# Kernel optimization log

Hardware: AMD Instinct MI355X
Metric: run time of the kernel (lower is better)

## Reference

```python
import jax, jax.numpy as jnp
import numpy as np

N_QUBITS = 4
N_LAYERS = 2
DIM = 2 ** N_QUBITS
B, S, E = 4, 512, 512


def _apply_ry_batched(state, theta, wire):
    # per-element RY data-encoding; state: [N, 2,2,2,2], theta: [N]
    ax = wire + 1
    half = theta * 0.5
    bshape = (-1,) + (1,) * (N_QUBITS - 1)
    c = jnp.cos(half).reshape(bshape)
    s = jnp.sin(half).reshape(bshape)
    s0 = jnp.take(state, 0, axis=ax)
    s1 = jnp.take(state, 1, axis=ax)
    return jnp.stack([c * s0 - s * s1, s * s0 + c * s1], axis=ax)


def _rot_gate(w3):
    # combined RZ(c) @ RY(b) @ RX(a), 2x2 complex (applied RX first)
    a, b, c = w3[0] * 0.5, w3[1] * 0.5, w3[2] * 0.5
    ca, sa = jnp.cos(a), jnp.sin(a)
    cb, sb = jnp.cos(b), jnp.sin(b)
    RX = jnp.array([[ca + 0j, -1j * sa], [-1j * sa, ca + 0j]])
    RY = jnp.array([[cb + 0j, -sb + 0j], [sb + 0j, cb + 0j]])
    ez = jnp.exp(-1j * c)
    RZ = jnp.array([[ez, 0j], [0j, jnp.conj(ez)]])
    return (RZ @ RY @ RX).astype(jnp.complex64)


def _apply_gate(state, gate, wire):
    s = jnp.tensordot(state, gate, axes=([wire + 1], [1]))
    return jnp.moveaxis(s, -1, wire + 1)


def _apply_cnot(state, ctrl, tgt):
    s = jnp.moveaxis(state, (ctrl + 1, tgt + 1), (1, 2))
    s = jnp.stack([s[:, 0], s[:, 1, ::-1]], axis=1)
    return jnp.moveaxis(s, (1, 2), (ctrl + 1, tgt + 1))


def _quantum_scores(angles, weights):
    # angles: [N, N_QUBITS] real; returns [N] = sum_i <Z_i>
    n = angles.shape[0]
    state = jnp.zeros((n, DIM), jnp.complex64).at[:, 0].set(1.0)
    state = state.reshape((n,) + (2,) * N_QUBITS)
    for w in range(N_QUBITS):
        state = _apply_ry_batched(state, angles[:, w], w)
    wmat = weights.reshape(N_LAYERS, N_QUBITS, 3)
    for layer in range(N_LAYERS):
        for w in range(N_QUBITS):
            state = _apply_gate(state, _rot_gate(wmat[layer, w]), w)
        for w in range(N_QUBITS - 1):
            state = _apply_cnot(state, w, w + 1)
        if N_QUBITS > 2:
            state = _apply_cnot(state, N_QUBITS - 1, 0)
    probs = (state.real ** 2 + state.imag ** 2).reshape(n, DIM)
    idx = np.arange(DIM)
    bits = (idx[:, None] >> np.arange(N_QUBITS)) & 1  # [DIM, n_qubits]
    zvec = jnp.asarray((1 - 2 * bits).sum(axis=1), jnp.float32)  # sum_i (-1)^bit_i
    return probs @ zvec


def setup_inputs() -> dict:
    key = jax.random.key(0)
    ks = jax.random.split(key, 8)
    x = jax.random.normal(ks[0], (B, S, E), jnp.float32)
    def lin(kk, fi, fo):
        return jax.random.normal(kk, (fi, fo), jnp.float32) / np.sqrt(fi)
    Wq = lin(ks[1], E, N_QUBITS)
    Wk = lin(ks[2], E, N_QUBITS)
    Wv = lin(ks[3], E, N_QUBITS)
    Wout = lin(ks[4], N_QUBITS, E)
    bq = 0.1 * jax.random.normal(ks[5], (N_QUBITS,), jnp.float32)
    bk = 0.1 * jax.random.normal(ks[6], (N_QUBITS,), jnp.float32)
    bv = jnp.zeros((N_QUBITS,), jnp.float32)
    bout = jnp.zeros((E,), jnp.float32)
    quantum_weights = 0.1 * jax.random.normal(ks[7], (N_LAYERS * N_QUBITS * 3,), jnp.float32)
    return {"x": x, "Wq": Wq, "bq": bq, "Wk": Wk, "bk": bk, "Wv": Wv, "bv": bv,
            "quantum_weights": quantum_weights, "Wout": Wout, "bout": bout}


def reference(x, Wq, bq, Wk, bk, Wv, bv, quantum_weights, Wout, bout):
    b, s, e = x.shape
    q = jnp.tanh(x @ Wq + bq)          # [B,S,nq]
    k = jnp.tanh(x @ Wk + bk)          # [B,S,nq]
    v = x @ Wv + bv                    # [B,S,nq]
    # pairwise circuit inputs: tanh(q_i + k_j) for all (b,i,j)
    angles = jnp.tanh(q[:, :, None, :] + k[:, None, :, :]).reshape(-1, N_QUBITS)
    scores = _quantum_scores(angles, quantum_weights).reshape(b, s, s)
    attn = jax.nn.softmax(scores / np.sqrt(N_QUBITS), axis=-1)
    attended = jnp.einsum('bij,bjd->bid', attn, v)
    out = attended @ Wout + bout       # [B,S,E]
    return out, attn
```

## Files before the change

kernel.cpp:

```cpp
#include <hip/hip_runtime.h>
#include <math.h>

#define NQ 4
#define DIM 16
#define BB 4
#define SS 512
#define EE 512
#define ROWS (BB * SS)

__global__ __launch_bounds__(256) void k_prep(
    const float* __restrict__ x,
    const float* __restrict__ Wq, const float* __restrict__ bq,
    const float* __restrict__ Wk, const float* __restrict__ bk,
    const float* __restrict__ Wv, const float* __restrict__ bv,
    const float* __restrict__ qw,
    float* __restrict__ tq, float* __restrict__ tk, float* __restrict__ v,
    float* __restrict__ T_out) {
    if (blockIdx.x == 0) {
        __shared__ float sG[8][8];
        __shared__ float Ur[DIM][DIM];
        __shared__ float Ui[DIM][DIM];
        __shared__ float sMr[256];
        int t = threadIdx.x;
        if (t < 8) {
            float a = qw[t * 3 + 0] * 0.5f;
            float b = qw[t * 3 + 1] * 0.5f;
            float c = qw[t * 3 + 2] * 0.5f;
            float sa = __sinf(a), ca = __cosf(a);
            float sb = __sinf(b), cb = __cosf(b);
            float sc = __sinf(c), cc = __cosf(c);
            float m00r = cb * ca, m00i = sb * sa;
            float m01r = -sb * ca, m01i = -cb * sa;
            float m10r = sb * ca, m10i = -cb * sa;
            float m11r = cb * ca, m11i = -sb * sa;
            sG[t][0] = cc * m00r + sc * m00i;
            sG[t][1] = cc * m00i - sc * m00r;
            sG[t][2] = cc * m01r + sc * m01i;
            sG[t][3] = cc * m01i - sc * m01r;
            sG[t][4] = cc * m10r - sc * m10i;
            sG[t][5] = cc * m10i + sc * m10r;
            sG[t][6] = cc * m11r - sc * m11i;
            sG[t][7] = cc * m11i + sc * m11r;
        }
        __syncthreads();
        if (t < DIM) {
            float vr[DIM], vi[DIM];
#pragma unroll
            for (int i = 0; i < DIM; ++i) { vr[i] = (i == t) ? 1.f : 0.f; vi[i] = 0.f; }
#pragma unroll
            for (int gi = 0; gi < 8; ++gi) {
                int w = gi & 3;
                float g00r = sG[gi][0], g00i = sG[gi][1];
                float g01r = sG[gi][2], g01i = sG[gi][3];
                float g10r = sG[gi][4], g10i = sG[gi][5];
                float g11r = sG[gi][6], g11i = sG[gi][7];
                int mask = 1 << (3 - w);
#pragma unroll
                for (int idx = 0; idx < DIM; ++idx) {
                    if (idx & mask) continue;
                    int i1 = idx | mask;
                    float r0 = vr[idx], i0 = vi[idx], r1 = vr[i1], i1v = vi[i1];
                    vr[idx] = g00r * r0 - g00i * i0 + g01r * r1 - g01i * i1v;
                    vi[idx] = g00r * i0 + g00i * r0 + g01r * i1v + g01i * r1;
                    vr[i1]  = g10r * r0 - g10i * i0 + g11r * r1 - g11i * i1v;
                    vi[i1]  = g10r * i0 + g10i * r0 + g11r * i1v + g11i * r1;
                }
                if (w == 3) {
                    const int cwire[4] = {0, 1, 2, 3};
                    const int twire[4] = {1, 2, 3, 0};
#pragma unroll
                    for (int e = 0; e < 4; ++e) {
                        int cmask = 1 << (3 - cwire[e]);
                        int tmask = 1 << (3 - twire[e]);
                        float nr[DIM], ni[DIM];
#pragma unroll
                        for (int idx = 0; idx < DIM; ++idx) {
                            int src = (idx & cmask) ? (idx ^ tmask) : idx;
                            nr[idx] = vr[src]; ni[idx] = vi[src];
                        }
#pragma unroll
                        for (int idx = 0; idx < DIM; ++idx) { vr[idx] = nr[idx]; vi[idx] = ni[idx]; }
                    }
                }
            }
#pragma unroll
            for (int i = 0; i < DIM; ++i) { Ur[i][t] = vr[i]; Ui[i][t] = vi[i]; }
        }
        __syncthreads();
        {
            int k = t >> 4, l = t & 15;
            float acc = 0.f;
#pragma unroll
            for (int idx = 0; idx < DIM; ++idx) {
                float z = 4.f - 2.f * (float)__popc(idx);
                acc += z * (Ur[idx][k] * Ur[idx][l] + Ui[idx][k] * Ui[idx][l]);
            }
            sMr[t] = acc;
        }
        __syncthreads();
        if (t < 81) {
            int e3 = t % 3, e2 = (t / 3) % 3, e1 = (t / 9) % 3, e0 = t / 27;
            int xm = ((e0 == 2) << 3) | ((e1 == 2) << 2) | ((e2 == 2) << 1) | (int)(e3 == 2);
            int sm = ((e0 == 1) << 3) | ((e1 == 1) << 2) | ((e2 == 1) << 1) | (int)(e3 == 1);
            float acc = 0.f;
#pragma unroll
            for (int K = 0; K < DIM; ++K) {
                float s = (__popc(K & sm) & 1) ? -1.f : 1.f;
                acc += s * sMr[K * 16 + (K ^ xm)];
            }
            T_out[((e0 * 3 + e1) * 3 + e2) * 4 + e3] = acc * (1.f / 32.f);
        }
        if (t < 27) T_out[t * 4 + 3] = 0.f;
    } else {
        int row = (blockIdx.x - 1) * 4 + (threadIdx.x >> 6);
        int lane = threadIdx.x & 63;
        const float4* xr4 = (const float4*)(x + (size_t)row * EE);
        float aq[4] = {0, 0, 0, 0}, ak[4] = {0, 0, 0, 0}, av[4] = {0, 0, 0, 0};
#pragma unroll
        for (int h = 0; h < 2; ++h) {
            int e4 = lane + h * 64;
            float4 xv = xr4[e4];
            float xc[4] = {xv.x, xv.y, xv.z, xv.w};
#pragma unroll
            for (int c = 0; c < 4; ++c) {
                int e = e4 * 4 + c;
                float4 wq = *(const float4*)(Wq + e * 4);
                float4 wk = *(const float4*)(Wk + e * 4);
                float4 wv = *(const float4*)(Wv + e * 4);
                aq[0] = fmaf(xc[c], wq.x, aq[0]); aq[1] = fmaf(xc[c], wq.y, aq[1]);
                aq[2] = fmaf(xc[c], wq.z, aq[2]); aq[3] = fmaf(xc[c], wq.w, aq[3]);
                ak[0] = fmaf(xc[c], wk.x, ak[0]); ak[1] = fmaf(xc[c], wk.y, ak[1]);
                ak[2] = fmaf(xc[c], wk.z, ak[2]); ak[3] = fmaf(xc[c], wk.w, ak[3]);
                av[0] = fmaf(xc[c], wv.x, av[0]); av[1] = fmaf(xc[c], wv.y, av[1]);
                av[2] = fmaf(xc[c], wv.z, av[2]); av[3] = fmaf(xc[c], wv.w, av[3]);
            }
        }
#pragma unroll
        for (int off = 32; off > 0; off >>= 1) {
#pragma unroll
            for (int c = 0; c < 4; ++c) {
                aq[c] += __shfl_down(aq[c], off, 64);
                ak[c] += __shfl_down(ak[c], off, 64);
                av[c] += __shfl_down(av[c], off, 64);
            }
        }
        if (lane == 0) {
#pragma unroll
            for (int c = 0; c < 4; ++c) {
                tq[row * 4 + c] = tanhf(tanhf(aq[c] + bq[c]));
                tk[row * 4 + c] = tanhf(tanhf(ak[c] + bk[c]));
                v[row * 4 + c] = av[c] + bv[c];
            }
        }
    }
}

__global__ __launch_bounds__(256) void k_attn(
    const float* __restrict__ tq, const float* __restrict__ tk,
    const float* __restrict__ v, const float* __restrict__ Tg,
    const float* __restrict__ Wout, const float* __restrict__ bout,
    float* __restrict__ attn_out, float* __restrict__ out) {
    int row = blockIdx.x;
    int b = row >> 9;
    int tid = threadIdx.x;
    int wid = tid >> 6, lane = tid & 63;
    int j0 = tid, j1 = tid + 256;

    __shared__ float4 sT[27];
    __shared__ float red[4][5];

    if (tid < 27) sT[tid] = ((const float4*)Tg)[tid];
    __syncthreads();

    const float4 q4 = *(const float4*)(tq + row * 4);
    const float4 ka = *(const float4*)(tk + (size_t)(b * SS + j0) * 4);
    const float4 kb = *(const float4*)(tk + (size_t)(b * SS + j1) * 4);

    float t0a = (q4.x + ka.x) / fmaf(q4.x, ka.x, 1.f);
    float t1a = (q4.y + ka.y) / fmaf(q4.y, ka.y, 1.f);
    float t2a = (q4.z + ka.z) / fmaf(q4.z, ka.z, 1.f);
    float t3a = (q4.w + ka.w) / fmaf(q4.w, ka.w, 1.f);
    float t0b = (q4.x + kb.x) / fmaf(q4.x, kb.x, 1.f);
    float t1b = (q4.y + kb.y) / fmaf(q4.y, kb.y, 1.f);
    float t2b = (q4.z + kb.z) / fmaf(q4.z, kb.z, 1.f);
    float t3b = (q4.w + kb.w) / fmaf(q4.w, kb.w, 1.f);

    float c0a = __cosf(t0a), s0a = __sinf(t0a);
    float c1a = __cosf(t1a), s1a = __sinf(t1a);
    float c2a = __cosf(t2a), s2a = __sinf(t2a);
    float c3a = __cosf(t3a), s3a = __sinf(t3a);
    float c0b = __cosf(t0b), s0b = __sinf(t0b);
    float c1b = __cosf(t1b), s1b = __sinf(t1b);
    float c2b = __cosf(t2b), s2b = __sinf(t2b);
    float c3b = __cosf(t3b), s3b = __sinf(t3b);

    float u0a[3] = {1.f, c0a, s0a}, u1a[3] = {1.f, c1a, s1a}, u2a[3] = {1.f, c2a, s2a};
    float u0b[3] = {1.f, c0b, s0b}, u1b[3] = {1.f, c1b, s1b}, u2b[3] = {1.f, c2b, s2b};

    float sc_a = 0.f, sc_b = 0.f;
#pragma unroll
    for (int e0 = 0; e0 < 3; ++e0) {
        float a1a = 0.f, a1b = 0.f;
#pragma unroll
        for (int e1 = 0; e1 < 3; ++e1) {
            float a2a = 0.f, a2b = 0.f;
#pragma unroll
            for (int e2 = 0; e2 < 3; ++e2) {
                float4 Tv = sT[(e0 * 3 + e1) * 3 + e2];
                float ia = fmaf(s3a, Tv.z, fmaf(c3a, Tv.y, Tv.x));
                float ib = fmaf(s3b, Tv.z, fmaf(c3b, Tv.y, Tv.x));
                a2a = fmaf(u2a[e2], ia, a2a);
                a2b = fmaf(u2b[e2], ib, a2b);
            }
            a1a = fmaf(u1a[e1], a2a, a1a);
            a1b = fmaf(u1b[e1], a2b, a1b);
        }
        sc_a = fmaf(u0a[e0], a1a, sc_a);
        sc_b = fmaf(u0b[e0], a1b, sc_b);
    }

    float ex_a = __expf(sc_a);
    float ex_b = __expf(sc_b);

    const float4 va = *(const float4*)(v + (size_t)(b * SS + j0) * 4);
    const float4 vb = *(const float4*)(v + (size_t)(b * SS + j1) * 4);
    float vals[5];
    vals[0] = ex_a + ex_b;
    vals[1] = fmaf(ex_a, va.x, ex_b * vb.x);
    vals[2] = fmaf(ex_a, va.y, ex_b * vb.y);
    vals[3] = fmaf(ex_a, va.z, ex_b * vb.z);
    vals[4] = fmaf(ex_a, va.w, ex_b * vb.w);
#pragma unroll
    for (int off = 32; off > 0; off >>= 1) {
#pragma unroll
        for (int c = 0; c < 5; ++c) vals[c] += __shfl_xor(vals[c], off, 64);
    }
    if (lane == 0) {
#pragma unroll
        for (int c = 0; c < 5; ++c) red[wid][c] = vals[c];
    }
    __syncthreads();

    float tot = red[0][0] + red[1][0] + red[2][0] + red[3][0];
    float inv = 1.f / tot;

    attn_out[(size_t)row * SS + j0] = ex_a * inv;
    attn_out[(size_t)row * SS + j1] = ex_b * inv;

    float a0 = (red[0][1] + red[1][1] + red[2][1] + red[3][1]) * inv;
    float a1 = (red[0][2] + red[1][2] + red[2][2] + red[3][2]) * inv;
    float a2 = (red[0][3] + red[1][3] + red[2][3] + red[3][3]) * inv;
    float a3 = (red[0][4] + red[1][4] + red[2][4] + red[3][4]) * inv;

    int e = tid * 2;
    float2 w0 = *(const float2*)(Wout + 0 * EE + e);
    float2 w1 = *(const float2*)(Wout + 1 * EE + e);
    float2 w2 = *(const float2*)(Wout + 2 * EE + e);
    float2 w3 = *(const float2*)(Wout + 3 * EE + e);
    float2 bb = *(const float2*)(bout + e);
    float2 o;
    o.x = fmaf(a0, w0.x, fmaf(a1, w1.x, fmaf(a2, w2.x, fmaf(a3, w3.x, bb.x))));
    o.y = fmaf(a0, w0.y, fmaf(a1, w1.y, fmaf(a2, w2.y, fmaf(a3, w3.y, bb.y))));
    *(float2*)(out + (size_t)row * EE + e) = o;
}

extern "C" void kernel_launch(void* const* d_in, const int* in_sizes, int n_in,
                              void* d_out, int out_size, void* d_ws, size_t ws_size,
                              hipStream_t stream) {
    const float* x    = (const float*)d_in[0];
    const float* Wq   = (const float*)d_in[1];
    const float* bq   = (const float*)d_in[2];
    const float* Wk   = (const float*)d_in[3];
    const float* bk   = (const float*)d_in[4];
    const float* Wv   = (const float*)d_in[5];
    const float* bv   = (const float*)d_in[6];
    const float* qw   = (const float*)d_in[7];
    const float* Wout = (const float*)d_in[8];
    const float* bout = (const float*)d_in[9];

    float* out  = (float*)d_out;
    float* attn = out + (size_t)ROWS * EE;

    float* ws  = (float*)d_ws;
    float* T   = ws;
    float* tq  = ws + 128;
    float* tk  = tq + ROWS * 4;
    float* v   = tk + ROWS * 4;

    k_prep<<<1 + ROWS / 4, 256, 0, stream>>>(x, Wq, bq, Wk, bk, Wv, bv, qw, tq, tk, v, T);
    k_attn<<<ROWS, 256, 0, stream>>>(tq, tk, v, T, Wout, bout, attn, out);
}
```

Before: 89.97 us.

## Use packed fp32 math, fast reciprocal/tanh, and read T coefficients directly

Packs the paired a/b score evaluations and the projection accumulators into 2-wide float vectors so the compiler can emit packed FMA instructions. Full divisions become hardware reciprocal multiplies, and tanhf becomes an exp/rcp approximation. The shared-memory staging of the T coefficient table and its barrier are dropped in favour of direct uniform global loads. This trades some accuracy and relies on scalar/cached loads to stay cheap.

```diff
diff --git a/kernel.cpp b/kernel.cpp
--- a/kernel.cpp
+++ b/kernel.cpp
@@ -7,6 +7,13 @@
 #define SS 512
 #define EE 512
 #define ROWS (BB * SS)
+
+typedef float f32x2 __attribute__((ext_vector_type(2)));
+
+__device__ __forceinline__ float fast_tanh(float x) {
+    float e = __expf(2.f * x);
+    return fmaf(-2.f, __builtin_amdgcn_rcpf(e + 1.f), 1.f);
+}
 
 __global__ __launch_bounds__(256) void k_prep(
     const float* __restrict__ x,
@@ -115,7 +122,9 @@
         int row = (blockIdx.x - 1) * 4 + (threadIdx.x >> 6);
         int lane = threadIdx.x & 63;
         const float4* xr4 = (const float4*)(x + (size_t)row * EE);
-        float aq[4] = {0, 0, 0, 0}, ak[4] = {0, 0, 0, 0}, av[4] = {0, 0, 0, 0};
+        f32x2 aq0 = {0.f, 0.f}, aq1 = {0.f, 0.f};
+        f32x2 ak0 = {0.f, 0.f}, ak1 = {0.f, 0.f};
+        f32x2 av0 = {0.f, 0.f}, av1 = {0.f, 0.f};
 #pragma unroll
         for (int h = 0; h < 2; ++h) {
             int e4 = lane + h * 64;
@@ -124,33 +133,38 @@
 #pragma unroll
             for (int c = 0; c < 4; ++c) {
                 int e = e4 * 4 + c;
-                float4 wq = *(const float4*)(Wq + e * 4);
-                float4 wk = *(const float4*)(Wk + e * 4);
-                float4 wv = *(const float4*)(Wv + e * 4);
-                aq[0] = fmaf(xc[c], wq.x, aq[0]); aq[1] = fmaf(xc[c], wq.y, aq[1]);
-                aq[2] = fmaf(xc[c], wq.z, aq[2]); aq[3] = fmaf(xc[c], wq.w, aq[3]);
-                ak[0] = fmaf(xc[c], wk.x, ak[0]); ak[1] = fmaf(xc[c], wk.y, ak[1]);
-                ak[2] = fmaf(xc[c], wk.z, ak[2]); ak[3] = fmaf(xc[c], wk.w, ak[3]);
-                av[0] = fmaf(xc[c], wv.x, av[0]); av[1] = fmaf(xc[c], wv.y, av[1]);
-                av[2] = fmaf(xc[c], wv.z, av[2]); av[3] = fmaf(xc[c], wv.w, av[3]);
+                const f32x2* wq2 = (const f32x2*)(Wq + e * 4);
+                const f32x2* wk2 = (const f32x2*)(Wk + e * 4);
+                const f32x2* wv2 = (const f32x2*)(Wv + e * 4);
+                f32x2 xb = {xc[c], xc[c]};
+                aq0 += xb * wq2[0]; aq1 += xb * wq2[1];
+                ak0 += xb * wk2[0]; ak1 += xb * wk2[1];
+                av0 += xb * wv2[0]; av1 += xb * wv2[1];
             }
         }
 #pragma unroll
         for (int off = 32; off > 0; off >>= 1) {
-#pragma unroll
-            for (int c = 0; c < 4; ++c) {
-                aq[c] += __shfl_down(aq[c], off, 64);
-                ak[c] += __shfl_down(ak[c], off, 64);
-                av[c] += __shfl_down(av[c], off, 64);
-            }
+            f32x2 t;
+            t.x = __shfl_down(aq0.x, off, 64); t.y = __shfl_down(aq0.y, off, 64); aq0 += t;
+            t.x = __shfl_down(aq1.x, off, 64); t.y = __shfl_down(aq1.y, off, 64); aq1 += t;
+            t.x = __shfl_down(ak0.x, off, 64); t.y = __shfl_down(ak0.y, off, 64); ak0 += t;
+            t.x = __shfl_down(ak1.x, off, 64); t.y = __shfl_down(ak1.y, off, 64); ak1 += t;
+            t.x = __shfl_down(av0.x, off, 64); t.y = __shfl_down(av0.y, off, 64); av0 += t;
+            t.x = __shfl_down(av1.x, off, 64); t.y = __shfl_down(av1.y, off, 64); av1 += t;
         }
         if (lane == 0) {
-#pragma unroll
-            for (int c = 0; c < 4; ++c) {
-                tq[row * 4 + c] = tanhf(tanhf(aq[c] + bq[c]));
-                tk[row * 4 + c] = tanhf(tanhf(ak[c] + bk[c]));
-                v[row * 4 + c] = av[c] + bv[c];
-            }
+            tq[row * 4 + 0] = fast_tanh(fast_tanh(aq0.x + bq[0]));
+            tq[row * 4 + 1] = fast_tanh(fast_tanh(aq0.y + bq[1]));
+            tq[row * 4 + 2] = fast_tanh(fast_tanh(aq1.x + bq[2]));
+            tq[row * 4 + 3] = fast_tanh(fast_tanh(aq1.y + bq[3]));
+            tk[row * 4 + 0] = fast_tanh(fast_tanh(ak0.x + bk[0]));
+            tk[row * 4 + 1] = fast_tanh(fast_tanh(ak0.y + bk[1]));
+            tk[row * 4 + 2] = fast_tanh(fast_tanh(ak1.x + bk[2]));
+            tk[row * 4 + 3] = fast_tanh(fast_tanh(ak1.y + bk[3]));
+            v[row * 4 + 0] = av0.x + bv[0];
+            v[row * 4 + 1] = av0.y + bv[1];
+            v[row * 4 + 2] = av1.x + bv[2];
+            v[row * 4 + 3] = av1.y + bv[3];
         }
     }
 }
@@ -166,61 +180,55 @@
     int wid = tid >> 6, lane = tid & 63;
     int j0 = tid, j1 = tid + 256;
 
-    __shared__ float4 sT[27];
     __shared__ float red[4][5];
-
-    if (tid < 27) sT[tid] = ((const float4*)Tg)[tid];
-    __syncthreads();
 
     const float4 q4 = *(const float4*)(tq + row * 4);
     const float4 ka = *(const float4*)(tk + (size_t)(b * SS + j0) * 4);
     const float4 kb = *(const float4*)(tk + (size_t)(b * SS + j1) * 4);
 
-    float t0a = (q4.x + ka.x) / fmaf(q4.x, ka.x, 1.f);
-    float t1a = (q4.y + ka.y) / fmaf(q4.y, ka.y, 1.f);
-    float t2a = (q4.z + ka.z) / fmaf(q4.z, ka.z, 1.f);
-    float t3a = (q4.w + ka.w) / fmaf(q4.w, ka.w, 1.f);
-    float t0b = (q4.x + kb.x) / fmaf(q4.x, kb.x, 1.f);
-    float t1b = (q4.y + kb.y) / fmaf(q4.y, kb.y, 1.f);
-    float t2b = (q4.z + kb.z) / fmaf(q4.z, kb.z, 1.f);
-    float t3b = (q4.w + kb.w) / fmaf(q4.w, kb.w, 1.f);
-
-    float c0a = __cosf(t0a), s0a = __sinf(t0a);
-    float c1a = __cosf(t1a), s1a = __sinf(t1a);
-    float c2a = __cosf(t2a), s2a = __sinf(t2a);
-    float c3a = __cosf(t3a), s3a = __sinf(t3a);
-    float c0b = __cosf(t0b), s0b = __sinf(t0b);
-    float c1b = __cosf(t1b), s1b = __sinf(t1b);
-    float c2b = __cosf(t2b), s2b = __sinf(t2b);
-    float c3b = __cosf(t3b), s3b = __sinf(t3b);
-
-    float u0a[3] = {1.f, c0a, s0a}, u1a[3] = {1.f, c1a, s1a}, u2a[3] = {1.f, c2a, s2a};
-    float u0b[3] = {1.f, c0b, s0b}, u1b[3] = {1.f, c1b, s1b}, u2b[3] = {1.f, c2b, s2b};
-
-    float sc_a = 0.f, sc_b = 0.f;
+    float t0a = (q4.x + ka.x) * __builtin_amdgcn_rcpf(fmaf(q4.x, ka.x, 1.f));
+    float t1a = (q4.y + ka.y) * __builtin_amdgcn_rcpf(fmaf(q4.y, ka.y, 1.f));
+    float t2a = (q4.z + ka.z) * __builtin_amdgcn_rcpf(fmaf(q4.z, ka.z, 1.f));
+    float t3a = (q4.w + ka.w) * __builtin_amdgcn_rcpf(fmaf(q4.w, ka.w, 1.f));
+    float t0b = (q4.x + kb.x) * __builtin_amdgcn_rcpf(fmaf(q4.x, kb.x, 1.f));
+    float t1b = (q4.y + kb.y) * __builtin_amdgcn_rcpf(fmaf(q4.y, kb.y, 1.f));
+    float t2b = (q4.z + kb.z) * __builtin_amdgcn_rcpf(fmaf(q4.z, kb.z, 1.f));
+    float t3b = (q4.w + kb.w) * __builtin_amdgcn_rcpf(fmaf(q4.w, kb.w, 1.f));
+
+    f32x2 u0[3], u1[3], u2[3];
+    u0[0] = (f32x2){1.f, 1.f}; u1[0] = (f32x2){1.f, 1.f}; u2[0] = (f32x2){1.f, 1.f};
+    u0[1] = (f32x2){__cosf(t0a), __cosf(t0b)};
+    u0[2] = (f32x2){__sinf(t0a), __sinf(t0b)};
+    u1[1] = (f32x2){__cosf(t1a), __cosf(t1b)};
+    u1[2] = (f32x2){__sinf(t1a), __sinf(t1b)};
+    u2[1] = (f32x2){__cosf(t2a), __cosf(t2b)};
+    u2[2] = (f32x2){__sinf(t2a), __sinf(t2b)};
+    f32x2 c3 = (f32x2){__cosf(t3a), __cosf(t3b)};
+    f32x2 s3 = (f32x2){__sinf(t3a), __sinf(t3b)};
+
+    f32x2 sc = {0.f, 0.f};
 #pragma unroll
     for (int e0 = 0; e0 < 3; ++e0) {
-        float a1a = 0.f, a1b = 0.f;
+        f32x2 a1 = {0.f, 0.f};
 #pragma unroll
         for (int e1 = 0; e1 < 3; ++e1) {
-            float a2a = 0.f, a2b = 0.f;
+            f32x2 a2 = {0.f, 0.f};
 #pragma unroll
             for (int e2 = 0; e2 < 3; ++e2) {
-                float4 Tv = sT[(e0 * 3 + e1) * 3 + e2];
-                float ia = fmaf(s3a, Tv.z, fmaf(c3a, Tv.y, Tv.x));
-                float ib = fmaf(s3b, Tv.z, fmaf(c3b, Tv.y, Tv.x));
-                a2a = fmaf(u2a[e2], ia, a2a);
-                a2b = fmaf(u2b[e2], ib, a2b);
-            }
-            a1a = fmaf(u1a[e1], a2a, a1a);
-            a1b = fmaf(u1b[e1], a2b, a1b);
-        }
-        sc_a = fmaf(u0a[e0], a1a, sc_a);
-        sc_b = fmaf(u0b[e0], a1b, sc_b);
+                int idx = ((e0 * 3 + e1) * 3 + e2) * 4;
+                float Tx = Tg[idx + 0];
+                float Ty = Tg[idx + 1];
+                float Tz = Tg[idx + 2];
+                f32x2 ia = (f32x2){Tx, Tx} + c3 * (f32x2){Ty, Ty} + s3 * (f32x2){Tz, Tz};
+                a2 += u2[e2] * ia;
+            }
+            a1 += u1[e1] * a2;
+        }
+        sc += u0[e0] * a1;
     }
 
-    float ex_a = __expf(sc_a);
-    float ex_b = __expf(sc_b);
+    float ex_a = __expf(sc.x);
+    float ex_b = __expf(sc.y);
 
     const float4 va = *(const float4*)(v + (size_t)(b * SS + j0) * 4);
     const float4 vb = *(const float4*)(v + (size_t)(b * SS + j1) * 4);
```

Result: faster. 84.91 us (-5.6%).
